# Kernel tuning notes

Hardware: AMD Instinct MI355X
Metric: run time of the kernel (lower is better)

The kernel has to match this reference:

```python
import jax, jax.numpy as jnp
import numpy as np

NUM_EMBEDDINGS = 512
EMBEDDING_DIM = 64
COMMITMENT_COST = 0.25


def setup_inputs() -> dict:
    key = jax.random.key(0)
    k1, k2 = jax.random.split(key)
    inputs = jax.random.normal(k1, (32, EMBEDDING_DIM, 64, 64), dtype=jnp.float32)
    embedding = jax.random.normal(k2, (NUM_EMBEDDINGS, EMBEDDING_DIM), dtype=jnp.float32)
    return {"inputs": inputs, "embedding": embedding}


def reference(inputs, embedding):
    # inputs: [B, C, H, W] with C == embedding_dim; embedding: [K, C]
    B, C, H, W = inputs.shape
    K = embedding.shape[0]
    x = jnp.transpose(inputs, (0, 2, 3, 1))          # [B, H, W, C]
    flat = x.reshape(-1, C)                          # [N, C], N = B*H*W
    N = flat.shape[0]
    distances = (
        jnp.sum(flat * flat, axis=1, keepdims=True)
        + jnp.sum(embedding * embedding, axis=1)
        - 2.0 * jnp.matmul(flat, embedding.T)
    )
    encoding_indices = jnp.argmin(distances, axis=1)  # [N]
    # quantized via gather (equivalent to one-hot @ embedding)
    quantized = embedding[encoding_indices].reshape(B, H, W, C)
    e_latent_loss = jnp.mean((jax.lax.stop_gradient(quantized) - x) ** 2)
    loss = COMMITMENT_COST * e_latent_loss
    # avg_probs = mean of one-hot encodings = normalized histogram of indices
    counts = jnp.zeros((K,), dtype=distances.dtype).at[encoding_indices].add(1.0)
    avg_probs = counts / N
    perplexity = jnp.exp(-jnp.sum(avg_probs * jnp.log(avg_probs + 1e-10)))
    encoding_indices_out = encoding_indices.reshape(B, 1, H, W)
    # source sets quantized=None before returning; return the three live outputs
    return loss, perplexity, encoding_indices_out
```

## Files before the change

### kernel.cpp

```cpp
#include <hip/hip_runtime.h>
#include <math.h>

#define KCODES 512
#define CDIM   64
#define HWPIX  4096
#define NPIX   131072
#define BLKPX  256
#define COMMIT 0.25f
#define TAU    0.01f

typedef __attribute__((ext_vector_type(8))) short s16x8;
typedef __attribute__((ext_vector_type(4))) float f32x4;

static __device__ __forceinline__ unsigned short f2bf(float f) {
    unsigned u = __float_as_uint(f);
    u += ((u >> 16) & 1u) + 0x7fffu;
    return (unsigned short)(u >> 16);
}
static __device__ __forceinline__ float bf2f(unsigned short h) {
    return __uint_as_float(((unsigned)h) << 16);
}

__global__ void vq_prep(const float* __restrict__ emb, float* __restrict__ ws) {
    int k = threadIdx.x;
    if (k < KCODES) {
        const float* e = emb + k * CDIM;
        double s = 0.0;
#pragma unroll
        for (int c = 0; c < CDIM; ++c) s += (double)e[c] * (double)e[c];
        ws[k] = (float)s;
        ((unsigned*)ws)[KCODES + k] = 0u;
    }
}

__launch_bounds__(256)
__global__ void vq_main(const float* __restrict__ in, const float* __restrict__ emb,
                        float* __restrict__ ws, float* __restrict__ out) {
    __shared__ __align__(16) short ehi[8192];
    __shared__ __align__(16) short elo[8192];
    __shared__ __align__(16) float e2s[KCODES];
    __shared__ unsigned hist[KCODES];
    __shared__ float ls_loss[BLKPX];
    __shared__ int   ls_idx[BLKPX];
    __shared__ float ls_gap[BLKPX];
    __shared__ int wl[BLKPX];
    __shared__ int wlc;
    __shared__ double rdd[256];
    __shared__ int    rdi[256];

    const int tid  = threadIdx.x;
    const int lane = tid & 63;
    const int wv   = tid >> 6;
    const int lg   = lane >> 4;
    const int li   = lane & 15;
    const int blk  = blockIdx.x;
    const int n0   = blk * BLKPX;
    const int b    = n0 >> 12;
    const int hwp0 = (n0 & 4095) + wv * 64 + li;
    const float* xb = in + (size_t)b * CDIM * HWPIX;

    for (int i = tid; i < KCODES; i += 256) { e2s[i] = ws[i]; hist[i] = 0u; }
    if (tid == 0) wlc = 0;

    float x2p[4];
    s16x8 xh[4][2], xl[4][2];
#pragma unroll
    for (int g = 0; g < 4; ++g) {
        float xr[16];
#pragma unroll
        for (int ks = 0; ks < 2; ++ks)
#pragma unroll
            for (int i = 0; i < 8; ++i)
                xr[ks * 8 + i] = xb[(ks * 32 + lg * 8 + i) * HWPIX + hwp0 + g * 16];
        float s = 0.f;
#pragma unroll
        for (int ks = 0; ks < 2; ++ks) {
            s16x8 h, l;
#pragma unroll
            for (int i = 0; i < 8; ++i) {
                float v = xr[ks * 8 + i];
                s += v * v;
                float m = -2.f * v;
                unsigned short hb = f2bf(m);
                h[i] = (short)hb;
                l[i] = (short)f2bf(m - bf2f(hb));
            }
            xh[g][ks] = h; xl[g][ks] = l;
        }
        x2p[g] = s;
    }

    float b1[4], b2[4]; int k1[4];
#pragma unroll
    for (int g = 0; g < 4; ++g) { b1[g] = 1e30f; b2[g] = 1e30f; k1[g] = 0; }

    for (int ch = 0; ch < 4; ++ch) {
#pragma unroll
        for (int s4 = 0; s4 < 4; ++s4) {
            int seg  = tid + 256 * s4;
            int code = seg >> 3;
            int cg   = seg & 7;
            const float* ep = emb + (ch * 128 + code) * CDIM + cg * 8;
            float4 fa = *(const float4*)(ep);
            float4 fb = *(const float4*)(ep + 4);
            float vv[8] = {fa.x, fa.y, fa.z, fa.w, fb.x, fb.y, fb.z, fb.w};
            s16x8 hh, ll;
#pragma unroll
            for (int i = 0; i < 8; ++i) {
                unsigned short hb = f2bf(vv[i]);
                hh[i] = (short)hb;
                ll[i] = (short)f2bf(vv[i] - bf2f(hb));
            }
            int off = (((code >> 4) * 2 + (cg >> 2)) * 16 + (code & 15)) * 32 + (cg & 3) * 8;
            *(s16x8*)&ehi[off] = hh;
            *(s16x8*)&elo[off] = ll;
        }
        __syncthreads();

#pragma unroll 2
        for (int t = 0; t < 8; ++t) {
            const int kb = ch * 128 + t * 16 + lg * 4;
            f32x4 e2v = *(f32x4*)&e2s[kb];
            const int ab = (t * 2) * 512 + li * 32 + lg * 8;
            s16x8 ah0 = *(s16x8*)&ehi[ab];
            s16x8 ah1 = *(s16x8*)&ehi[ab + 512];
            s16x8 al0 = *(s16x8*)&elo[ab];
            s16x8 al1 = *(s16x8*)&elo[ab + 512];
#pragma unroll
            for (int g = 0; g < 4; ++g) {
                f32x4 acc = e2v;
                acc = __builtin_amdgcn_mfma_f32_16x16x32_bf16(ah0, xh[g][0], acc, 0, 0, 0);
                acc = __builtin_amdgcn_mfma_f32_16x16x32_bf16(ah1, xh[g][1], acc, 0, 0, 0);
                acc = __builtin_amdgcn_mfma_f32_16x16x32_bf16(ah0, xl[g][0], acc, 0, 0, 0);
                acc = __builtin_amdgcn_mfma_f32_16x16x32_bf16(ah1, xl[g][1], acc, 0, 0, 0);
                acc = __builtin_amdgcn_mfma_f32_16x16x32_bf16(al0, xh[g][0], acc, 0, 0, 0);
                acc = __builtin_amdgcn_mfma_f32_16x16x32_bf16(al1, xh[g][1], acc, 0, 0, 0);
#pragma unroll
                for (int j = 0; j < 4; ++j) {
                    float d = acc[j];
                    int k = kb + j;
                    float nb2 = fminf(fmaxf(d, b1[g]), b2[g]);
                    bool take = d < b1[g];
                    b1[g] = take ? d : b1[g];
                    k1[g] = take ? k : k1[g];
                    b2[g] = nb2;
                }
            }
        }
        __syncthreads();
    }

#pragma unroll
    for (int g = 0; g < 4; ++g) {
#pragma unroll
        for (int m = 16; m <= 32; m <<= 1) {
            float ob1 = __shfl_xor(b1[g], m, 64);
            float ob2 = __shfl_xor(b2[g], m, 64);
            int   ok1 = __shfl_xor(k1[g], m, 64);
            float nb2 = fminf(fminf(b2[g], ob2), fmaxf(b1[g], ob1));
            bool take = (ob1 < b1[g]) || (ob1 == b1[g] && ok1 < k1[g]);
            b1[g] = take ? ob1 : b1[g];
            k1[g] = take ? ok1 : k1[g];
            b2[g] = nb2;
            x2p[g] += __shfl_xor(x2p[g], m, 64);
        }
    }

    if (lane < 16) {
#pragma unroll
        for (int g = 0; g < 4; ++g) {
            int p = wv * 64 + g * 16 + lane;
            ls_idx[p]  = k1[g];
            ls_loss[p] = x2p[g] + b1[g];
            ls_gap[p]  = b2[g] - b1[g];
        }
    }
    __syncthreads();

    if (tid < BLKPX && ls_gap[tid] <= TAU) { int w = atomicAdd(&wlc, 1); wl[w] = tid; }
    __syncthreads();

    const int nfl = wlc;
    for (int w = 0; w < nfl; ++w) {
        const int p   = wl[w];
        const int hwp = (n0 & 4095) + p;
        double bd = 1e300; int bi = 0;
#pragma unroll
        for (int kk = 0; kk < 2; ++kk) {
            int k = tid * 2 + kk;
            const float* e = emb + k * CDIM;
            double s = 0.0;
            for (int c = 0; c < CDIM; ++c) {
                double t = (double)xb[c * HWPIX + hwp] - (double)e[c];
                s += t * t;
            }
            if (s < bd) { bd = s; bi = k; }
        }
        rdd[tid] = bd; rdi[tid] = bi;
        __syncthreads();
        for (int s = 128; s > 0; s >>= 1) {
            if (tid < s) {
                double od = rdd[tid + s]; int oi = rdi[tid + s];
                if (od < rdd[tid] || (od == rdd[tid] && oi < rdi[tid])) { rdd[tid] = od; rdi[tid] = oi; }
            }
            __syncthreads();
        }
        if (tid == 0) { ls_idx[p] = rdi[0]; ls_loss[p] = (float)rdd[0]; }
        __syncthreads();
    }

    if (tid < BLKPX) {
        int k = ls_idx[tid];
        out[2 + n0 + tid] = (float)k;
        atomicAdd(&hist[k], 1u);
    }
    __syncthreads();
    for (int s = 128; s > 0; s >>= 1) {
        if (tid < s) ls_loss[tid] += ls_loss[tid + s];
        __syncthreads();
    }
    if (tid == 0) ws[2 * KCODES + blk] = ls_loss[0];

    unsigned* counts = ((unsigned*)ws) + KCODES;
    for (int i = tid; i < KCODES; i += 256) {
        unsigned v = hist[i];
        if (v) atomicAdd(&counts[i], v);
    }
}

__global__ void vq_final(const float* __restrict__ ws, float* __restrict__ out) {
    __shared__ float red[KCODES];
    int t = threadIdx.x;

    red[t] = ws[2 * KCODES + t];
    __syncthreads();
    for (int s = 256; s > 0; s >>= 1) {
        if (t < s) red[t] += red[t + s];
        __syncthreads();
    }
    float loss_sum = red[0];
    __syncthreads();

    unsigned cnt = ((const unsigned*)ws)[KCODES + t];
    float p = (float)cnt / (float)NPIX;
    red[t] = p * logf(p + 1e-10f);
    __syncthreads();
    for (int s = 256; s > 0; s >>= 1) {
        if (t < s) red[t] += red[t + s];
        __syncthreads();
    }
    if (t == 0) {
        out[0] = COMMIT * loss_sum / ((float)NPIX * (float)CDIM);
        out[1] = expf(-red[0]);
    }
}

extern "C" void kernel_launch(void* const* d_in, const int* in_sizes, int n_in,
                              void* d_out, int out_size, void* d_ws, size_t ws_size,
                              hipStream_t stream) {
    const float* in  = (const float*)d_in[0];
    const float* emb = (const float*)d_in[1];
    float* out = (float*)d_out;
    float* ws  = (float*)d_ws;

    vq_prep<<<1, KCODES, 0, stream>>>(emb, ws);
    vq_main<<<NPIX / BLKPX, 256, 0, stream>>>(in, emb, ws, out);
    vq_final<<<1, KCODES, 0, stream>>>(ws, out);
}
```

Baseline: 65.19 us.

## Precompute split-bf16 codebook in prep kernel and split codes across waves

The prep kernel now converts the codebook into hi/lo bf16 MFMA fragments in workspace once, so the main kernel streams them from global with register prefetch instead of converting into LDS per block. Block size halves to 128 pixels, with two waves per pixel group each covering half the codes. The argmin tracking packs distance and index into one unsigned key with integer min, and the per-block histogram becomes direct global atomics. This trades a larger fp64 fallback threshold (more refinement pixels) and masked distance precision for lower per-block conversion and LDS overhead.

```diff
diff --git a/kernel.cpp b/kernel.cpp
--- a/kernel.cpp
+++ b/kernel.cpp
@@ -5,12 +5,18 @@
 #define CDIM   64
 #define HWPIX  4096
 #define NPIX   131072
-#define BLKPX  256
+#define BLKPX  128
+#define NBLK   (NPIX / BLKPX)
 #define COMMIT 0.25f
-#define TAU    0.01f
+#define TAU    0.125f
+#define CB_OFF 8192
 
 typedef __attribute__((ext_vector_type(8))) short s16x8;
 typedef __attribute__((ext_vector_type(4))) float f32x4;
+typedef __attribute__((ext_vector_type(4))) unsigned u32x4;
+
+static __device__ __forceinline__ unsigned umin_(unsigned a, unsigned b) { return a < b ? a : b; }
+static __device__ __forceinline__ unsigned umax_(unsigned a, unsigned b) { return a > b ? a : b; }
 
 static __device__ __forceinline__ unsigned short f2bf(float f) {
     unsigned u = __float_as_uint(f);
@@ -20,187 +26,211 @@
 static __device__ __forceinline__ float bf2f(unsigned short h) {
     return __uint_as_float(((unsigned)h) << 16);
 }
+static __device__ __forceinline__ unsigned cvt_pk_bf16(float a, float b) {
+    unsigned r;
+    asm("v_cvt_pk_bf16_f32 %0, %1, %2" : "=v"(r) : "v"(a), "v"(b));
+    return r;
+}
 
 __global__ void vq_prep(const float* __restrict__ emb, float* __restrict__ ws) {
-    int k = threadIdx.x;
-    if (k < KCODES) {
-        const float* e = emb + k * CDIM;
-        double s = 0.0;
-#pragma unroll
-        for (int c = 0; c < CDIM; ++c) s += (double)e[c] * (double)e[c];
-        ws[k] = (float)s;
-        ((unsigned*)ws)[KCODES + k] = 0u;
-    }
-}
-
-__launch_bounds__(256)
-__global__ void vq_main(const float* __restrict__ in, const float* __restrict__ emb,
-                        float* __restrict__ ws, float* __restrict__ out) {
-    __shared__ __align__(16) short ehi[8192];
-    __shared__ __align__(16) short elo[8192];
-    __shared__ __align__(16) float e2s[KCODES];
-    __shared__ unsigned hist[KCODES];
-    __shared__ float ls_loss[BLKPX];
-    __shared__ int   ls_idx[BLKPX];
-    __shared__ float ls_gap[BLKPX];
-    __shared__ int wl[BLKPX];
-    __shared__ int wlc;
-    __shared__ double rdd[256];
-    __shared__ int    rdi[256];
+    int k = blockIdx.x * 256 + threadIdx.x;
+    const float* e = emb + k * CDIM;
+    float v[CDIM];
+    double s = 0.0;
+#pragma unroll
+    for (int c = 0; c < CDIM; ++c) { v[c] = e[c]; s += (double)v[c] * (double)v[c]; }
+    ws[k] = (float)s;
+    ((unsigned*)ws)[KCODES + k] = 0u;
+
+    unsigned char* base = (unsigned char*)ws + CB_OFF + (k >> 4) * 4096;
+    const int row = k & 15;
+#pragma unroll
+    for (int ks = 0; ks < 2; ++ks) {
+#pragma unroll
+        for (int lg = 0; lg < 4; ++lg) {
+            s16x8 hh, ll;
+#pragma unroll
+            for (int i = 0; i < 8; ++i) {
+                float f = v[ks * 32 + lg * 8 + i];
+                unsigned short hb = f2bf(f);
+                hh[i] = (short)hb;
+                ll[i] = (short)f2bf(f - bf2f(hb));
+            }
+            int off = (lg * 16 + row) * 16;
+            *(s16x8*)(base + ks * 1024 + off)        = hh;
+            *(s16x8*)(base + 2048 + ks * 1024 + off) = ll;
+        }
+    }
+}
+
+__global__ __launch_bounds__(256)
+void vq_main(const float* __restrict__ in, const float* __restrict__ emb,
+             float* __restrict__ ws, float* __restrict__ out) {
+    __shared__ float    e2s[KCODES];
+    __shared__ unsigned mk1[2][BLKPX];
+    __shared__ unsigned mk2[2][BLKPX];
+    __shared__ int      ls_idx[BLKPX];
+    __shared__ float    ls_loss[BLKPX];
+    __shared__ int      wl[BLKPX];
+    __shared__ int      wlc;
+    __shared__ float    wsum[4];
+    __shared__ double   rdd[256];
+    __shared__ int      rdi[256];
 
     const int tid  = threadIdx.x;
     const int lane = tid & 63;
     const int wv   = tid >> 6;
+    const int ch   = wv & 1;
+    const int ph   = wv >> 1;
     const int lg   = lane >> 4;
     const int li   = lane & 15;
     const int blk  = blockIdx.x;
     const int n0   = blk * BLKPX;
-    const int b    = n0 >> 12;
-    const int hwp0 = (n0 & 4095) + wv * 64 + li;
-    const float* xb = in + (size_t)b * CDIM * HWPIX;
-
-    for (int i = tid; i < KCODES; i += 256) { e2s[i] = ws[i]; hist[i] = 0u; }
+    const int hw0  = n0 & 4095;
+    const float* xb = in + (size_t)(n0 >> 12) * CDIM * HWPIX;
+
+    e2s[tid]       = ws[tid];
+    e2s[tid + 256] = ws[tid + 256];
     if (tid == 0) wlc = 0;
 
-    float x2p[4];
+    float x2p1[4];
     s16x8 xh[4][2], xl[4][2];
+    const int hwb = hw0 + ph * 64 + li;
 #pragma unroll
     for (int g = 0; g < 4; ++g) {
-        float xr[16];
+        float vv[16];
 #pragma unroll
         for (int ks = 0; ks < 2; ++ks)
 #pragma unroll
             for (int i = 0; i < 8; ++i)
-                xr[ks * 8 + i] = xb[(ks * 32 + lg * 8 + i) * HWPIX + hwp0 + g * 16];
+                vv[ks * 8 + i] = xb[(ks * 32 + lg * 8 + i) * HWPIX + hwb + g * 16];
         float s = 0.f;
 #pragma unroll
+        for (int j = 0; j < 16; ++j) s += vv[j] * vv[j];
+#pragma unroll
         for (int ks = 0; ks < 2; ++ks) {
-            s16x8 h, l;
-#pragma unroll
-            for (int i = 0; i < 8; ++i) {
-                float v = xr[ks * 8 + i];
-                s += v * v;
-                float m = -2.f * v;
-                unsigned short hb = f2bf(m);
-                h[i] = (short)hb;
-                l[i] = (short)f2bf(m - bf2f(hb));
-            }
-            xh[g][ks] = h; xl[g][ks] = l;
-        }
-        x2p[g] = s;
-    }
-
-    float b1[4], b2[4]; int k1[4];
-#pragma unroll
-    for (int g = 0; g < 4; ++g) { b1[g] = 1e30f; b2[g] = 1e30f; k1[g] = 0; }
-
-    for (int ch = 0; ch < 4; ++ch) {
-#pragma unroll
-        for (int s4 = 0; s4 < 4; ++s4) {
-            int seg  = tid + 256 * s4;
-            int code = seg >> 3;
-            int cg   = seg & 7;
-            const float* ep = emb + (ch * 128 + code) * CDIM + cg * 8;
-            float4 fa = *(const float4*)(ep);
-            float4 fb = *(const float4*)(ep + 4);
-            float vv[8] = {fa.x, fa.y, fa.z, fa.w, fb.x, fb.y, fb.z, fb.w};
-            s16x8 hh, ll;
-#pragma unroll
-            for (int i = 0; i < 8; ++i) {
-                unsigned short hb = f2bf(vv[i]);
-                hh[i] = (short)hb;
-                ll[i] = (short)f2bf(vv[i] - bf2f(hb));
-            }
-            int off = (((code >> 4) * 2 + (cg >> 2)) * 16 + (code & 15)) * 32 + (cg & 3) * 8;
-            *(s16x8*)&ehi[off] = hh;
-            *(s16x8*)&elo[off] = ll;
-        }
-        __syncthreads();
-
-#pragma unroll 2
-        for (int t = 0; t < 8; ++t) {
-            const int kb = ch * 128 + t * 16 + lg * 4;
-            f32x4 e2v = *(f32x4*)&e2s[kb];
-            const int ab = (t * 2) * 512 + li * 32 + lg * 8;
-            s16x8 ah0 = *(s16x8*)&ehi[ab];
-            s16x8 ah1 = *(s16x8*)&ehi[ab + 512];
-            s16x8 al0 = *(s16x8*)&elo[ab];
-            s16x8 al1 = *(s16x8*)&elo[ab + 512];
-#pragma unroll
-            for (int g = 0; g < 4; ++g) {
-                f32x4 acc = e2v;
-                acc = __builtin_amdgcn_mfma_f32_16x16x32_bf16(ah0, xh[g][0], acc, 0, 0, 0);
-                acc = __builtin_amdgcn_mfma_f32_16x16x32_bf16(ah1, xh[g][1], acc, 0, 0, 0);
-                acc = __builtin_amdgcn_mfma_f32_16x16x32_bf16(ah0, xl[g][0], acc, 0, 0, 0);
-                acc = __builtin_amdgcn_mfma_f32_16x16x32_bf16(ah1, xl[g][1], acc, 0, 0, 0);
-                acc = __builtin_amdgcn_mfma_f32_16x16x32_bf16(al0, xh[g][0], acc, 0, 0, 0);
-                acc = __builtin_amdgcn_mfma_f32_16x16x32_bf16(al1, xh[g][1], acc, 0, 0, 0);
-#pragma unroll
-                for (int j = 0; j < 4; ++j) {
-                    float d = acc[j];
-                    int k = kb + j;
-                    float nb2 = fminf(fmaxf(d, b1[g]), b2[g]);
-                    bool take = d < b1[g];
-                    b1[g] = take ? d : b1[g];
-                    k1[g] = take ? k : k1[g];
-                    b2[g] = nb2;
-                }
-            }
-        }
-        __syncthreads();
-    }
-
+            unsigned hws[4], lws[4];
+#pragma unroll
+            for (int p2 = 0; p2 < 4; ++p2) {
+                float m0 = -2.f * vv[ks * 8 + 2 * p2];
+                float m1 = -2.f * vv[ks * 8 + 2 * p2 + 1];
+                unsigned h = cvt_pk_bf16(m0, m1);
+                float h0 = __uint_as_float(h << 16);
+                float h1 = __uint_as_float(h & 0xFFFF0000u);
+                hws[p2] = h;
+                lws[p2] = cvt_pk_bf16(m0 - h0, m1 - h1);
+            }
+            xh[g][ks] = __builtin_bit_cast(s16x8, (u32x4){hws[0], hws[1], hws[2], hws[3]});
+            xl[g][ks] = __builtin_bit_cast(s16x8, (u32x4){lws[0], lws[1], lws[2], lws[3]});
+        }
+        x2p1[g] = s;
+    }
 #pragma unroll
     for (int g = 0; g < 4; ++g) {
+        x2p1[g] += __shfl_xor(x2p1[g], 16, 64);
+        x2p1[g] += __shfl_xor(x2p1[g], 32, 64);
+        x2p1[g] += 1.0f;
+    }
+    __syncthreads();
+
+    const unsigned char* cb = (const unsigned char*)ws + CB_OFF + ch * 65536 + lane * 16;
+    unsigned b1[4] = {~0u, ~0u, ~0u, ~0u};
+    unsigned b2[4] = {~0u, ~0u, ~0u, ~0u};
+
+    s16x8 nah0 = *(const s16x8*)(cb);
+    s16x8 nah1 = *(const s16x8*)(cb + 1024);
+    s16x8 nal0 = *(const s16x8*)(cb + 2048);
+    s16x8 nal1 = *(const s16x8*)(cb + 3072);
+#pragma unroll
+    for (int t = 0; t < 16; ++t) {
+        s16x8 ah0 = nah0, ah1 = nah1, al0 = nal0, al1 = nal1;
+        if (t < 15) {
+            const unsigned char* nb = cb + (t + 1) * 4096;
+            nah0 = *(const s16x8*)(nb);
+            nah1 = *(const s16x8*)(nb + 1024);
+            nal0 = *(const s16x8*)(nb + 2048);
+            nal1 = *(const s16x8*)(nb + 3072);
+        }
+        const int kb = ch * 256 + t * 16 + lg * 4;
+        f32x4 e2v = *(const f32x4*)(e2s + kb);
+#pragma unroll
+        for (int g = 0; g < 4; ++g) {
+            f32x4 acc;
+            acc[0] = e2v[0] + x2p1[g];
+            acc[1] = e2v[1] + x2p1[g];
+            acc[2] = e2v[2] + x2p1[g];
+            acc[3] = e2v[3] + x2p1[g];
+            acc = __builtin_amdgcn_mfma_f32_16x16x32_bf16(ah0, xh[g][0], acc, 0, 0, 0);
+            acc = __builtin_amdgcn_mfma_f32_16x16x32_bf16(ah1, xh[g][1], acc, 0, 0, 0);
+            acc = __builtin_amdgcn_mfma_f32_16x16x32_bf16(ah0, xl[g][0], acc, 0, 0, 0);
+            acc = __builtin_amdgcn_mfma_f32_16x16x32_bf16(ah1, xl[g][1], acc, 0, 0, 0);
+            acc = __builtin_amdgcn_mfma_f32_16x16x32_bf16(al0, xh[g][0], acc, 0, 0, 0);
+            acc = __builtin_amdgcn_mfma_f32_16x16x32_bf16(al1, xh[g][1], acc, 0, 0, 0);
+            unsigned K0 = (__float_as_uint(acc[0]) & 0xFFFFFE00u) | (unsigned)(kb + 0);
+            unsigned K1 = (__float_as_uint(acc[1]) & 0xFFFFFE00u) | (unsigned)(kb + 1);
+            unsigned K2 = (__float_as_uint(acc[2]) & 0xFFFFFE00u) | (unsigned)(kb + 2);
+            unsigned K3 = (__float_as_uint(acc[3]) & 0xFFFFFE00u) | (unsigned)(kb + 3);
+            unsigned amin = umin_(K0, K1), amax = umax_(K0, K1);
+            unsigned bmin = umin_(K2, K3), bmax = umax_(K2, K3);
+            unsigned best = umin_(amin, bmin);
+            unsigned snd  = umin_(umax_(amin, bmin), umin_(amax, bmax));
+            b2[g] = umin_(umin_(b2[g], snd), umax_(b1[g], best));
+            b1[g] = umin_(b1[g], best);
+        }
+    }
+
+#pragma unroll
+    for (int g = 0; g < 4; ++g) {
 #pragma unroll
         for (int m = 16; m <= 32; m <<= 1) {
-            float ob1 = __shfl_xor(b1[g], m, 64);
-            float ob2 = __shfl_xor(b2[g], m, 64);
-            int   ok1 = __shfl_xor(k1[g], m, 64);
-            float nb2 = fminf(fminf(b2[g], ob2), fmaxf(b1[g], ob1));
-            bool take = (ob1 < b1[g]) || (ob1 == b1[g] && ok1 < k1[g]);
-            b1[g] = take ? ob1 : b1[g];
-            k1[g] = take ? ok1 : k1[g];
+            unsigned o1 = (unsigned)__shfl_xor((int)b1[g], m, 64);
+            unsigned o2 = (unsigned)__shfl_xor((int)b2[g], m, 64);
+            unsigned nb2 = umin_(umin_(b2[g], o2), umax_(b1[g], o1));
+            b1[g] = umin_(b1[g], o1);
             b2[g] = nb2;
-            x2p[g] += __shfl_xor(x2p[g], m, 64);
-        }
-    }
-
-    if (lane < 16) {
-#pragma unroll
-        for (int g = 0; g < 4; ++g) {
-            int p = wv * 64 + g * 16 + lane;
-            ls_idx[p]  = k1[g];
-            ls_loss[p] = x2p[g] + b1[g];
-            ls_gap[p]  = b2[g] - b1[g];
-        }
-    }
-    __syncthreads();
-
-    if (tid < BLKPX && ls_gap[tid] <= TAU) { int w = atomicAdd(&wlc, 1); wl[w] = tid; }
+        }
+        if (lane < 16) {
+            int p = ph * 64 + g * 16 + lane;
+            mk1[ch][p] = b1[g];
+            mk2[ch][p] = b2[g];
+        }
+    }
+    __syncthreads();
+
+    if (tid < BLKPX) {
+        unsigned a1 = mk1[0][tid], c1 = mk1[1][tid];
+        unsigned a2 = mk2[0][tid], c2 = mk2[1][tid];
+        unsigned K1 = umin_(a1, c1);
+        unsigned K2 = umin_(umax_(a1, c1), umin_(a2, c2));
+        ls_idx[tid]  = (int)(K1 & 511u);
+        float d1 = __uint_as_float(K1 & 0xFFFFFE00u);
+        float d2 = __uint_as_float(K2 & 0xFFFFFE00u);
+        ls_loss[tid] = d1 - 1.0f;
+        if (d2 - d1 <= TAU) { int w = atomicAdd(&wlc, 1); wl[w] = tid; }
+    }
     __syncthreads();
 
     const int nfl = wlc;
     for (int w = 0; w < nfl; ++w) {
-        const int p   = wl[w];
-        const int hwp = (n0 & 4095) + p;
+        const int p = wl[w];
+        const int hwp = hw0 + p;
         double bd = 1e300; int bi = 0;
 #pragma unroll
         for (int kk = 0; kk < 2; ++kk) {
             int k = tid * 2 + kk;
             const float* e = emb + k * CDIM;
             double s = 0.0;
-            for (int c = 0; c < CDIM; ++c) {
-                double t = (double)xb[c * HWPIX + hwp] - (double)e[c];
+            for (int cc = 0; cc < CDIM; ++cc) {
+                double t = (double)xb[cc * HWPIX + hwp] - (double)e[cc];
                 s += t * t;
             }
             if (s < bd) { bd = s; bi = k; }
         }
         rdd[tid] = bd; rdi[tid] = bi;
         __syncthreads();
-        for (int s = 128; s > 0; s >>= 1) {
-            if (tid < s) {
-                double od = rdd[tid + s]; int oi = rdi[tid + s];
+        for (int st = 128; st > 0; st >>= 1) {
+            if (tid < st) {
+                double od = rdd[tid + st]; int oi = rdi[tid + st];
                 if (od < rdd[tid] || (od == rdd[tid] && oi < rdi[tid])) { rdd[tid] = od; rdi[tid] = oi; }
             }
             __syncthreads();
@@ -209,30 +239,26 @@
         __syncthreads();
     }
 
+    unsigned* counts = ((unsigned*)ws) + KCODES;
     if (tid < BLKPX) {
         int k = ls_idx[tid];
         out[2 + n0 + tid] = (float)k;
-        atomicAdd(&hist[k], 1u);
-    }
-    __syncthreads();
-    for (int s = 128; s > 0; s >>= 1) {
-        if (tid < s) ls_loss[tid] += ls_loss[tid + s];
-        __syncthreads();
-    }
-    if (tid == 0) ws[2 * KCODES + blk] = ls_loss[0];
-
-    unsigned* counts = ((unsigned*)ws) + KCODES;
-    for (int i = tid; i < KCODES; i += 256) {
-        unsigned v = hist[i];
-        if (v) atomicAdd(&counts[i], v);
-    }
+        atomicAdd(&counts[k], 1u);
+    }
+    float lv = (tid < BLKPX) ? ls_loss[tid] : 0.f;
+#pragma unroll
+    for (int off = 32; off > 0; off >>= 1) lv += __shfl_down(lv, off, 64);
+    if (lane == 0) wsum[wv] = lv;
+    __syncthreads();
+    if (tid == 0)
+        ws[2 * KCODES + blk] = (wsum[0] + wsum[1]) + (wsum[2] + wsum[3]);
 }
 
 __global__ void vq_final(const float* __restrict__ ws, float* __restrict__ out) {
     __shared__ float red[KCODES];
     int t = threadIdx.x;
 
-    red[t] = ws[2 * KCODES + t];
+    red[t] = ws[2 * KCODES + t] + ws[2 * KCODES + 512 + t];
     __syncthreads();
     for (int s = 256; s > 0; s >>= 1) {
         if (t < s) red[t] += red[t + s];
@@ -263,7 +289,7 @@
     float* out = (float*)d_out;
     float* ws  = (float*)d_ws;
 
-    vq_prep<<<1, KCODES, 0, stream>>>(emb, ws);
-    vq_main<<<NPIX / BLKPX, 256, 0, stream>>>(in, emb, ws, out);
+    vq_prep<<<2, 256, 0, stream>>>(emb, ws);
+    vq_main<<<NBLK, 256, 0, stream>>>(in, emb, ws, out);
     vq_final<<<1, KCODES, 0, stream>>>(ws, out);
 }
```

New measurement: 175.6 us. +169.3%, slower.
